# Kernel optimization log

Measured on AMD Instinct MI355X. Metric: run time of the kernel, lower is better.

## Reference

```python
import jax, jax.numpy as jnp
import numpy as np

B, CIN, COUT, H, W = 8, 64, 64, 128, 128
HEADS, CR = 4, 32  # reduced_ch = CIN // 2
N = H * W


def build_grid_edges(P, Pw):
    """Directed 4-neighborhood grid edges + self loops, matching build_grid_edge_index."""
    src, dst = [], []
    for i in range(P):
        for j in range(Pw):
            u = i * Pw + j
            if i - 1 >= 0:
                src.append(u); dst.append((i - 1) * Pw + j)
            if i + 1 < P:
                src.append(u); dst.append((i + 1) * Pw + j)
            if j - 1 >= 0:
                src.append(u); dst.append(i * Pw + j - 1)
            if j + 1 < Pw:
                src.append(u); dst.append(i * Pw + j + 1)
            src.append(u); dst.append(u)
    return np.asarray(src, np.int32), np.asarray(dst, np.int32)


def setup_inputs() -> dict:
    key = jax.random.key(0)
    ks = jax.random.split(key, 6)
    src_np, dst_np = build_grid_edges(H, W)
    return {
        "x": jax.random.normal(ks[0], (B, CIN, H, W), jnp.float32),
        "w_reduce": jax.random.normal(ks[1], (CR, CIN), jnp.float32) * (1.0 / np.sqrt(CIN)),
        "w_lin": jax.random.normal(ks[2], (HEADS * CR, CR), jnp.float32) * (1.0 / np.sqrt(CR)),
        "att_src": jax.random.normal(ks[3], (HEADS, CR), jnp.float32) * 0.1,
        "att_dst": jax.random.normal(ks[4], (HEADS, CR), jnp.float32) * 0.1,
        "b_gat": jnp.zeros((CR,), jnp.float32),
        "w_restore": jax.random.normal(ks[5], (COUT, CR), jnp.float32) * (1.0 / np.sqrt(CR)),
        "bn_gamma": jnp.ones((COUT,), jnp.float32),
        "bn_beta": jnp.zeros((COUT,), jnp.float32),
        "src": jnp.asarray(src_np),
        "dst": jnp.asarray(dst_np),
    }


def reference(x, w_reduce, w_lin, att_src, att_dst, b_gat, w_restore, bn_gamma, bn_beta, src, dst):
    b, cin, h, w = x.shape
    heads, cr = att_src.shape
    n = h * w
    res = x  # residual is Identity since input_channels == output_channels

    xr = jnp.einsum('oc,bchw->bohw', w_reduce, x)          # 1x1 reduce conv
    nodes = xr.transpose(0, 2, 3, 1).reshape(b, n, cr)      # [B, N, Cr]

    def gat(nd):
        # PyG GATConv: lin -> per-edge attention -> segment softmax -> scatter sum -> head mean + bias
        hfeat = (nd @ w_lin.T).reshape(n, heads, cr)        # [N, H, Cr]
        a_s = jnp.sum(hfeat * att_src, axis=-1)             # [N, H]
        a_d = jnp.sum(hfeat * att_dst, axis=-1)             # [N, H]
        e = a_s[src] + a_d[dst]                             # [E, H]
        e = jnp.where(e > 0, e, 0.2 * e)                    # leaky_relu(0.2)
        emax = jax.ops.segment_max(e, dst, num_segments=n)  # softmax over incoming edges
        ex = jnp.exp(e - emax[dst])
        denom = jax.ops.segment_sum(ex, dst, num_segments=n)
        alpha = ex / denom[dst]                             # [E, H]
        msg = alpha[:, :, None] * hfeat[src]                # [E, H, Cr]
        agg = jax.ops.segment_sum(msg, dst, num_segments=n) # [N, H, Cr]
        return agg.mean(axis=1) + b_gat                     # concat=False -> head mean, + bias

    g = jax.vmap(gat)(nodes)                                # [B, N, Cr]
    g = g.reshape(b, h, w, cr).transpose(0, 3, 1, 2)

    out = jnp.einsum('oc,bchw->bohw', w_restore, g) + res   # 1x1 restore conv + residual

    # BatchNorm2d (training mode: batch statistics, biased variance)
    mean = out.mean(axis=(0, 2, 3), keepdims=True)
    var = out.var(axis=(0, 2, 3), keepdims=True)
    out = (out - mean) / jnp.sqrt(var + 1e-5)
    out = out * bn_gamma[None, :, None, None] + bn_beta[None, :, None, None]
    return jax.nn.relu(out)
```

## Files before the change

### kernel.cpp

```cpp
#include <hip/hip_runtime.h>

#define NN 16384
#define CINC 64

__global__ void gat_k0(const float* __restrict__ w_restore,
                       const float* __restrict__ b_gat,
                       const float* __restrict__ w_reduce,
                       const float* __restrict__ w_lin,
                       const float* __restrict__ att_src,
                       const float* __restrict__ att_dst,
                       float* __restrict__ rb, float* __restrict__ wredT,
                       float* __restrict__ S, float* __restrict__ D) {
    int t = threadIdx.x;
    if (t < 128) {
        int h = t >> 5, k = t & 31;
        float s = 0.f, d = 0.f;
        for (int c = 0; c < 32; ++c) {
            float wl = w_lin[(h * 32 + c) * 32 + k];
            s += att_src[h * 32 + c] * wl;
            d += att_dst[h * 32 + c] * wl;
        }
        S[t] = s; D[t] = d;
    } else if (t < 192) {
        int o = t - 128;
        float r = 0.f;
        for (int c = 0; c < 32; ++c) r += w_restore[o * 32 + c] * b_gat[c];
        rb[o] = r;
    }
    for (int idx = t; idx < 2048; idx += 256) {
        int k = idx & 31, c = idx >> 5;
        wredT[c * 32 + k] = w_reduce[k * 64 + c];
    }
}

__global__ __launch_bounds__(256) void gat_k1(
        const float* __restrict__ x, const float* __restrict__ wredT,
        const float* __restrict__ S, const float* __restrict__ D,
        float* __restrict__ red_g, float* __restrict__ as_ws,
        float* __restrict__ ad_ws) {
    __shared__ float xs[4096];
    __shared__ float red_lds[32][64];

    int tid = threadIdx.x;
    int s = blockIdx.x;
    int b = s >> 8;
    int v0 = (s & 255) << 6;

    const float* xb = x + (size_t)b * CINC * NN + v0;
    for (int idx = tid; idx < 4096; idx += 256) {
        int c = idx >> 6, nd = idx & 63;
        xs[idx] = xb[(size_t)c * NN + nd];
    }
    __syncthreads();

    int nd = tid & 63;
    int wv = __builtin_amdgcn_readfirstlane(tid >> 6);

    {
        float a0 = 0.f, a1 = 0.f, a2 = 0.f, a3 = 0.f,
              a4 = 0.f, a5 = 0.f, a6 = 0.f, a7 = 0.f;
        const float* wt = wredT + wv * 8;
#pragma unroll 4
        for (int c = 0; c < 64; ++c) {
            float xc = xs[c * 64 + nd];
            const float* w = wt + c * 32;
            a0 = fmaf(w[0], xc, a0);
            a1 = fmaf(w[1], xc, a1);
            a2 = fmaf(w[2], xc, a2);
            a3 = fmaf(w[3], xc, a3);
            a4 = fmaf(w[4], xc, a4);
            a5 = fmaf(w[5], xc, a5);
            a6 = fmaf(w[6], xc, a6);
            a7 = fmaf(w[7], xc, a7);
        }
        int k0 = wv * 8;
        float* rg = red_g + (size_t)b * 32 * NN + v0 + nd;
        red_lds[k0 + 0][nd] = a0; rg[(size_t)(k0 + 0) * NN] = a0;
        red_lds[k0 + 1][nd] = a1; rg[(size_t)(k0 + 1) * NN] = a1;
        red_lds[k0 + 2][nd] = a2; rg[(size_t)(k0 + 2) * NN] = a2;
        red_lds[k0 + 3][nd] = a3; rg[(size_t)(k0 + 3) * NN] = a3;
        red_lds[k0 + 4][nd] = a4; rg[(size_t)(k0 + 4) * NN] = a4;
        red_lds[k0 + 5][nd] = a5; rg[(size_t)(k0 + 5) * NN] = a5;
        red_lds[k0 + 6][nd] = a6; rg[(size_t)(k0 + 6) * NN] = a6;
        red_lds[k0 + 7][nd] = a7; rg[(size_t)(k0 + 7) * NN] = a7;
    }
    __syncthreads();

    {
        float rv[32];
#pragma unroll
        for (int k = 0; k < 32; ++k) rv[k] = red_lds[k][nd];
        const float* sp = S + wv * 32;
        const float* dp = D + wv * 32;
        float pas = 0.f, pad_ = 0.f;
#pragma unroll
        for (int k = 0; k < 32; ++k) {
            pas  = fmaf(sp[k], rv[k], pas);
            pad_ = fmaf(dp[k], rv[k], pad_);
        }
        as_ws[((size_t)b * 4 + wv) * NN + v0 + nd] = pas;
        ad_ws[((size_t)b * 4 + wv) * NN + v0 + nd] = pad_;
    }
}

__global__ __launch_bounds__(256) void gat_k2(
        const float* __restrict__ x, const float* __restrict__ w_lin,
        const float* __restrict__ w_restore, const float* __restrict__ rb,
        const float* __restrict__ red_g, const float* __restrict__ as_ws,
        const float* __restrict__ ad_ws, float* __restrict__ outp,
        float* __restrict__ part) {
    __shared__ float gp[4][8][64];
    __shared__ float gout[32][64];
    __shared__ float stat_lds[128];

    int tid = threadIdx.x;
    int s = blockIdx.x;
    int b = s >> 8;
    int v0 = (s & 255) << 6;
    int nd = tid & 63;
    int wv = __builtin_amdgcn_readfirstlane(tid >> 6);
    int v = v0 + nd;
    int i = v >> 7, j = v & 127;

    int un0 = v;
    int un1 = i > 0   ? v - 128 : v;
    int un2 = i < 127 ? v + 128 : v;
    int un3 = j > 0   ? v - 1   : v;
    int un4 = j < 127 ? v + 1   : v;

    float al[4][5];
#pragma unroll
    for (int h = 0; h < 4; ++h) {
        const float* asp = as_ws + ((size_t)b * 4 + h) * NN;
        float adv = ad_ws[((size_t)b * 4 + h) * NN + v];
        float e0 = asp[un0] + adv, e1 = asp[un1] + adv, e2 = asp[un2] + adv,
              e3 = asp[un3] + adv, e4 = asp[un4] + adv;
        e0 = e0 > 0.f ? e0 : 0.2f * e0;
        e1 = e1 > 0.f ? e1 : 0.2f * e1;
        e2 = e2 > 0.f ? e2 : 0.2f * e2;
        e3 = e3 > 0.f ? e3 : 0.2f * e3;
        e4 = e4 > 0.f ? e4 : 0.2f * e4;
        e1 += i > 0   ? 0.f : -1e30f;
        e2 += i < 127 ? 0.f : -1e30f;
        e3 += j > 0   ? 0.f : -1e30f;
        e4 += j < 127 ? 0.f : -1e30f;
        float m = fmaxf(fmaxf(fmaxf(e0, e1), fmaxf(e2, e3)), e4);
        e0 = __expf(e0 - m); e1 = __expf(e1 - m); e2 = __expf(e2 - m);
        e3 = __expf(e3 - m); e4 = __expf(e4 - m);
        float sc = 0.25f / (e0 + e1 + e2 + e3 + e4);
        al[h][0] = e0 * sc; al[h][1] = e1 * sc; al[h][2] = e2 * sc;
        al[h][3] = e3 * sc; al[h][4] = e4 * sc;
    }

    float gpart[32];
#pragma unroll
    for (int c = 0; c < 32; ++c) gpart[c] = 0.f;

    const float* rp = red_g + (size_t)b * 32 * NN + (size_t)(wv * 8) * NN;
    const float* wl = w_lin;
#pragma unroll 1
    for (int kc = 0; kc < 4; ++kc) {
        const float* rk0 = rp + (size_t)(kc * 2) * NN;
        const float* rk1 = rk0 + NN;
        float t00 = rk0[un0], t01 = rk0[un1], t02 = rk0[un2],
              t03 = rk0[un3], t04 = rk0[un4];
        float t10 = rk1[un0], t11 = rk1[un1], t12 = rk1[un2],
              t13 = rk1[un3], t14 = rk1[un4];
        float r0[4], r1[4];
#pragma unroll
        for (int h = 0; h < 4; ++h) {
            r0[h] = al[h][0] * t00 + al[h][1] * t01 + al[h][2] * t02 +
                    al[h][3] * t03 + al[h][4] * t04;
            r1[h] = al[h][0] * t10 + al[h][1] * t11 + al[h][2] * t12 +
                    al[h][3] * t13 + al[h][4] * t14;
        }
#pragma unroll
        for (int c = 0; c < 32; ++c) {
#pragma unroll
            for (int h = 0; h < 4; ++h) {
                const float* wk = wl + (h * 32 + c) * 32 + wv * 8 + kc * 2;
                gpart[c] += wk[0] * r0[h] + wk[1] * r1[h];
            }
        }
    }

#pragma unroll
    for (int q = 0; q < 4; ++q) {
#pragma unroll
        for (int cq = 0; cq < 8; ++cq) gp[wv][cq][nd] = gpart[q * 8 + cq];
        __syncthreads();
#pragma unroll
        for (int t2 = 0; t2 < 2; ++t2) {
            int cq = wv * 2 + t2;
            gout[q * 8 + cq][nd] = gp[0][cq][nd] + gp[1][cq][nd] +
                                   gp[2][cq][nd] + gp[3][cq][nd];
        }
        __syncthreads();
    }

    {
        float gv[32];
#pragma unroll
        for (int c = 0; c < 32; ++c) gv[c] = gout[c][nd];
        const float* xb = x + (size_t)b * CINC * NN + v0 + nd;
        float* ob = outp + (size_t)b * CINC * NN + v0 + nd;
        const float* wr_h = w_restore + (size_t)wv * 16 * 32;
#pragma unroll 2
        for (int o16 = 0; o16 < 16; ++o16) {
            int o = wv * 16 + o16;
            const float* wr = wr_h + o16 * 32;
            float acc = rb[o];
#pragma unroll
            for (int c = 0; c < 32; ++c)
                acc = fmaf(wr[c], gv[c], acc);
            acc += xb[(size_t)o * NN];
            ob[(size_t)o * NN] = acc;
            float r1 = acc, r2 = acc * acc;
#pragma unroll
            for (int off = 32; off > 0; off >>= 1) {
                r1 += __shfl_xor(r1, off, 64);
                r2 += __shfl_xor(r2, off, 64);
            }
            if (nd == 0) { stat_lds[o] = r1; stat_lds[64 + o] = r2; }
        }
    }
    __syncthreads();
    if (tid < 128) part[(size_t)s * 128 + tid] = stat_lds[tid];
}

__global__ __launch_bounds__(256) void gat_k2b(
        const float* __restrict__ part, float* __restrict__ stats) {
    __shared__ float red[4];
    int jj = blockIdx.x;
    int tid = threadIdx.x;
    float acc = 0.f;
    for (int s = tid; s < 2048; s += 256) acc += part[(size_t)s * 128 + jj];
#pragma unroll
    for (int off = 32; off > 0; off >>= 1) acc += __shfl_xor(acc, off, 64);
    int wv = tid >> 6, lane = tid & 63;
    if (lane == 0) red[wv] = acc;
    __syncthreads();
    if (tid == 0) stats[jj] = red[0] + red[1] + red[2] + red[3];
}

__global__ __launch_bounds__(256) void gat_k3(
        float* __restrict__ out, const float* __restrict__ stats,
        const float* __restrict__ gamma, const float* __restrict__ beta) {
    int f = blockIdx.x * 256 + threadIdx.x;
    int e = f * 4;
    int c = (e >> 14) & 63;
    const float cnt_inv = 1.f / 131072.f;
    float mean = stats[c] * cnt_inv;
    float var = stats[64 + c] * cnt_inv - mean * mean;
    float inv = rsqrtf(var + 1e-5f);
    float sc = gamma[c] * inv;
    float sh = beta[c] - mean * sc;
    float4 vv = reinterpret_cast<float4*>(out)[f];
    vv.x = fmaxf(vv.x * sc + sh, 0.f);
    vv.y = fmaxf(vv.y * sc + sh, 0.f);
    vv.z = fmaxf(vv.z * sc + sh, 0.f);
    vv.w = fmaxf(vv.w * sc + sh, 0.f);
    reinterpret_cast<float4*>(out)[f] = vv;
}

extern "C" void kernel_launch(void* const* d_in, const int* in_sizes, int n_in,
                              void* d_out, int out_size, void* d_ws, size_t ws_size,
                              hipStream_t stream) {
    const float* x         = (const float*)d_in[0];
    const float* w_reduce  = (const float*)d_in[1];
    const float* w_lin     = (const float*)d_in[2];
    const float* att_src   = (const float*)d_in[3];
    const float* att_dst   = (const float*)d_in[4];
    const float* b_gat     = (const float*)d_in[5];
    const float* w_restore = (const float*)d_in[6];
    const float* bn_gamma  = (const float*)d_in[7];
    const float* bn_beta   = (const float*)d_in[8];

    float* ws     = (float*)d_ws;
    float* red_g  = ws;
    float* as_ws  = red_g + 4194304;
    float* ad_ws  = as_ws + 524288;
    float* Sf     = ad_ws + 524288;
    float* Df     = Sf + 128;
    float* rbf    = Df + 128;
    float* wredT  = rbf + 64;
    float* stats  = wredT + 2048;
    float* part   = stats + 128;

    gat_k0<<<1, 256, 0, stream>>>(w_restore, b_gat, w_reduce, w_lin,
                                  att_src, att_dst, rbf, wredT, Sf, Df);
    gat_k1<<<2048, 256, 0, stream>>>(x, wredT, Sf, Df, red_g, as_ws, ad_ws);
    gat_k2<<<2048, 256, 0, stream>>>(x, w_lin, w_restore, rbf, red_g,
                                     as_ws, ad_ws, (float*)d_out, part);
    gat_k2b<<<128, 256, 0, stream>>>(part, stats);
    gat_k3<<<8192, 256, 0, stream>>>((float*)d_out, stats, bn_gamma, bn_beta);
}
```

Before: 103.0 us.

## Fuse GAT output, BN stats reduction and BN apply into a cooperative kernel

Replaces the three final launches (output/partials, stats reduction, BN+ReLU) with one cooperative kernel. Each block handles two strips, keeps the pre-BN output in LDS, and uses grid-wide syncs to reduce the statistics before applying BN and ReLU straight from LDS. This removes the global write and re-read of the pre-BN output and two launches. The cost is two grid barriers, about 33KB of LDS per block, and the need for 1024 blocks to be co-resident, with a fallback to the old path when that fails.

```diff
diff --git a/kernel.cpp b/kernel.cpp
--- a/kernel.cpp
+++ b/kernel.cpp
@@ -1,4 +1,7 @@
 #include <hip/hip_runtime.h>
+#include <hip/hip_cooperative_groups.h>
+
+namespace cg = cooperative_groups;
 
 #define NN 16384
 #define CINC 64
@@ -103,20 +106,18 @@
     }
 }
 
-__global__ __launch_bounds__(256) void gat_k2(
+__device__ __forceinline__ void process_strip(
+        int strip, int tid, float* region, float* stat_lds, bool first,
         const float* __restrict__ x, const float* __restrict__ w_lin,
         const float* __restrict__ w_restore, const float* __restrict__ rb,
         const float* __restrict__ red_g, const float* __restrict__ as_ws,
-        const float* __restrict__ ad_ws, float* __restrict__ outp,
-        float* __restrict__ part) {
-    __shared__ float gp[4][8][64];
-    __shared__ float gout[32][64];
-    __shared__ float stat_lds[128];
-
-    int tid = threadIdx.x;
-    int s = blockIdx.x;
-    int b = s >> 8;
-    int v0 = (s & 255) << 6;
+        const float* __restrict__ ad_ws) {
+    float (*gp)[8][64] = reinterpret_cast<float (*)[8][64]>(region);
+    float (*gout)[64]  = reinterpret_cast<float (*)[64]>(region + 2048);
+    float* lds_out     = region;
+
+    int b = strip >> 8;
+    int v0 = (strip & 255) << 6;
     int nd = tid & 63;
     int wv = __builtin_amdgcn_readfirstlane(tid >> 6);
     int v = v0 + nd;
@@ -184,6 +185,7 @@
         }
     }
 
+    __syncthreads();
 #pragma unroll
     for (int q = 0; q < 4; ++q) {
 #pragma unroll
@@ -202,8 +204,8 @@
         float gv[32];
 #pragma unroll
         for (int c = 0; c < 32; ++c) gv[c] = gout[c][nd];
+        __syncthreads();
         const float* xb = x + (size_t)b * CINC * NN + v0 + nd;
-        float* ob = outp + (size_t)b * CINC * NN + v0 + nd;
         const float* wr_h = w_restore + (size_t)wv * 16 * 32;
 #pragma unroll 2
         for (int o16 = 0; o16 < 16; ++o16) {
@@ -214,17 +216,118 @@
             for (int c = 0; c < 32; ++c)
                 acc = fmaf(wr[c], gv[c], acc);
             acc += xb[(size_t)o * NN];
-            ob[(size_t)o * NN] = acc;
+            lds_out[o16 * 256 + tid] = acc;
             float r1 = acc, r2 = acc * acc;
 #pragma unroll
             for (int off = 32; off > 0; off >>= 1) {
                 r1 += __shfl_xor(r1, off, 64);
                 r2 += __shfl_xor(r2, off, 64);
             }
-            if (nd == 0) { stat_lds[o] = r1; stat_lds[64 + o] = r2; }
-        }
-    }
-    __syncthreads();
+            if (nd == 0) {
+                if (first) { stat_lds[o] = r1; stat_lds[64 + o] = r2; }
+                else       { stat_lds[o] += r1; stat_lds[64 + o] += r2; }
+            }
+        }
+    }
+}
+
+__global__ __launch_bounds__(256, 4) void gat_k2f(
+        const float* __restrict__ x, const float* __restrict__ w_lin,
+        const float* __restrict__ w_restore, const float* __restrict__ rb,
+        const float* __restrict__ red_g, const float* __restrict__ as_ws,
+        const float* __restrict__ ad_ws, const float* __restrict__ gamma,
+        const float* __restrict__ beta, float* __restrict__ outp,
+        float* __restrict__ part, float* __restrict__ stats) {
+    __shared__ float regionA[4096];
+    __shared__ float regionB[4096];
+    __shared__ float stat_lds[128];
+    __shared__ float red4[4];
+
+    cg::grid_group grid = cg::this_grid();
+
+    int tid = threadIdx.x;
+    int bid = blockIdx.x;
+    int nd = tid & 63;
+    int wv = __builtin_amdgcn_readfirstlane(tid >> 6);
+
+    process_strip(bid * 2 + 0, tid, regionA, stat_lds, true,
+                  x, w_lin, w_restore, rb, red_g, as_ws, ad_ws);
+    __syncthreads();
+    process_strip(bid * 2 + 1, tid, regionB, stat_lds, false,
+                  x, w_lin, w_restore, rb, red_g, as_ws, ad_ws);
+    __syncthreads();
+    if (tid < 128)
+        __hip_atomic_store(&part[(size_t)bid * 128 + tid], stat_lds[tid],
+                           __ATOMIC_RELAXED, __HIP_MEMORY_SCOPE_AGENT);
+
+    grid.sync();
+
+    if (bid < 128) {
+        float acc = 0.f;
+        for (int q = tid; q < 1024; q += 256)
+            acc += __hip_atomic_load(&part[(size_t)q * 128 + bid],
+                                     __ATOMIC_RELAXED,
+                                     __HIP_MEMORY_SCOPE_AGENT);
+#pragma unroll
+        for (int off = 32; off > 0; off >>= 1) acc += __shfl_xor(acc, off, 64);
+        if (nd == 0) red4[wv] = acc;
+        __syncthreads();
+        if (tid == 0)
+            __hip_atomic_store(&stats[bid], red4[0] + red4[1] + red4[2] + red4[3],
+                               __ATOMIC_RELAXED, __HIP_MEMORY_SCOPE_AGENT);
+    }
+
+    grid.sync();
+
+    const float cnt_inv = 1.f / 131072.f;
+#pragma unroll
+    for (int sid = 0; sid < 2; ++sid) {
+        int strip = bid * 2 + sid;
+        int b = strip >> 8;
+        int v0 = (strip & 255) << 6;
+        float* region = sid ? regionB : regionA;
+        float* ob = outp + (size_t)b * CINC * NN + v0 + nd;
+#pragma unroll 2
+        for (int o16 = 0; o16 < 16; ++o16) {
+            int o = wv * 16 + o16;
+            float s1 = __hip_atomic_load(&stats[o], __ATOMIC_RELAXED,
+                                         __HIP_MEMORY_SCOPE_AGENT);
+            float s2 = __hip_atomic_load(&stats[64 + o], __ATOMIC_RELAXED,
+                                         __HIP_MEMORY_SCOPE_AGENT);
+            float mean = s1 * cnt_inv;
+            float var = s2 * cnt_inv - mean * mean;
+            float inv = rsqrtf(var + 1e-5f);
+            float sc = gamma[o] * inv;
+            float sh = beta[o] - mean * sc;
+            float val = region[o16 * 256 + tid];
+            ob[(size_t)o * NN] = fmaxf(val * sc + sh, 0.f);
+        }
+    }
+}
+
+__global__ __launch_bounds__(256) void gat_k2(
+        const float* __restrict__ x, const float* __restrict__ w_lin,
+        const float* __restrict__ w_restore, const float* __restrict__ rb,
+        const float* __restrict__ red_g, const float* __restrict__ as_ws,
+        const float* __restrict__ ad_ws, float* __restrict__ outp,
+        float* __restrict__ part) {
+    __shared__ float region[4096];
+    __shared__ float stat_lds[128];
+    int tid = threadIdx.x;
+    int s = blockIdx.x;
+    process_strip(s, tid, region, stat_lds, true,
+                  x, w_lin, w_restore, rb, red_g, as_ws, ad_ws);
+    __syncthreads();
+    int nd = tid & 63;
+    int wv = __builtin_amdgcn_readfirstlane(tid >> 6);
+    int b = s >> 8;
+    int v0 = (s & 255) << 6;
+    float* ob = outp + (size_t)b * CINC * NN + v0 + nd;
+#pragma unroll 2
+    for (int o16 = 0; o16 < 16; ++o16) {
+        int o = wv * 16 + o16;
+        ob[(size_t)o * NN] = region[o16 * 256 + tid];
+    }
     if (tid < 128) part[(size_t)s * 128 + tid] = stat_lds[tid];
 }
 
@@ -287,11 +390,32 @@
     float* stats  = wredT + 2048;
     float* part   = stats + 128;
 
+    float* outp = (float*)d_out;
+
     gat_k0<<<1, 256, 0, stream>>>(w_restore, b_gat, w_reduce, w_lin,
                                   att_src, att_dst, rbf, wredT, Sf, Df);
     gat_k1<<<2048, 256, 0, stream>>>(x, wredT, Sf, Df, red_g, as_ws, ad_ws);
-    gat_k2<<<2048, 256, 0, stream>>>(x, w_lin, w_restore, rbf, red_g,
-                                     as_ws, ad_ws, (float*)d_out, part);
-    gat_k2b<<<128, 256, 0, stream>>>(part, stats);
-    gat_k3<<<8192, 256, 0, stream>>>((float*)d_out, stats, bn_gamma, bn_beta);
-}
+
+    int dev = 0;
+    hipGetDevice(&dev);
+    int coop = 0, ncu = 0, maxB = 0;
+    hipDeviceGetAttribute(&coop, hipDeviceAttributeCooperativeLaunch, dev);
+    hipDeviceGetAttribute(&ncu, hipDeviceAttributeMultiprocessorCount, dev);
+    hipOccupancyMaxActiveBlocksPerMultiprocessor(&maxB, (const void*)gat_k2f,
+                                                 256, 0);
+    bool useCoop = coop && ((long)maxB * (long)ncu >= 1024L);
+
+    if (useCoop) {
+        void* args[] = { (void*)&x, (void*)&w_lin, (void*)&w_restore,
+                         (void*)&rbf, (void*)&red_g, (void*)&as_ws,
+                         (void*)&ad_ws, (void*)&bn_gamma, (void*)&bn_beta,
+                         (void*)&outp, (void*)&part, (void*)&stats };
+        hipLaunchCooperativeKernel((void*)gat_k2f, dim3(1024), dim3(256),
+                                   args, 0, stream);
+    } else {
+        gat_k2<<<2048, 256, 0, stream>>>(x, w_lin, w_restore, rbf, red_g,
+                                         as_ws, ad_ws, outp, part);
+        gat_k2b<<<128, 256, 0, stream>>>(part, stats);
+        gat_k3<<<8192, 256, 0, stream>>>(outp, stats, bn_gamma, bn_beta);
+    }
+}
```

Result: slower. 121.3 us (+17.8%).
